# Kernel optimization log

Measured on AMD Instinct MI355X. Metric: run time of the kernel, lower is better.

Reference implementation:

```python
import jax, jax.numpy as jnp
import numpy as np

N_NODES = 20000
N_EDGES = 640000
IN_F = 128
CL1_F = 128
CL2_F = 128
OUT_F = 2


def setup_inputs() -> dict:
    key = jax.random.key(0)
    ks = jax.random.split(key, 8)
    x = jax.random.normal(ks[0], (N_NODES, IN_F), dtype=jnp.float32)
    edge_index = jax.random.randint(ks[1], (2, N_EDGES), 0, N_NODES, dtype=jnp.int64)
    s1 = 1.0 / np.sqrt(IN_F)
    s2 = 1.0 / np.sqrt(CL1_F)
    s3 = 1.0 / np.sqrt(CL2_F)
    W1 = jax.random.uniform(ks[2], (IN_F, CL1_F), jnp.float32, -s1, s1)
    b1 = jax.random.uniform(ks[3], (CL1_F,), jnp.float32, -s1, s1)
    W2 = jax.random.uniform(ks[4], (CL1_F, CL2_F), jnp.float32, -s2, s2)
    b2 = jax.random.uniform(ks[5], (CL2_F,), jnp.float32, -s2, s2)
    W3 = jax.random.uniform(ks[6], (CL2_F, OUT_F), jnp.float32, -s3, s3)
    b3 = jax.random.uniform(ks[7], (OUT_F,), jnp.float32, -s3, s3)
    return {"x": x, "edge_index": edge_index, "W1": W1, "b1": b1,
            "W2": W2, "b2": b2, "W3": W3, "b3": b3}


def _scatter_mean(feat_src, src, dst, n_nodes):
    # out[i] = mean over edges e with dst[e]==i of feat_src gathered at src[e]
    msg = feat_src[src]                                   # [E, F] gather
    summed = jax.ops.segment_sum(msg, dst, num_segments=n_nodes)  # [N, F]
    ones = jnp.ones((src.shape[0],), dtype=feat_src.dtype)
    cnt = jax.ops.segment_sum(ones, dst, num_segments=n_nodes)    # [N]
    return summed / jnp.maximum(cnt, 1.0)[:, None]


def _mpnn_layer(x, src, dst, W, b, n_nodes):
    aggr = _scatter_mean(x, src, dst, n_nodes)
    return jax.nn.relu(aggr @ W + b)


def reference(x, edge_index, W1, b1, W2, b2, W3, b3):
    src, dst = edge_index[0], edge_index[1]
    n = x.shape[0]
    h = _mpnn_layer(x, src, dst, W1, b1, n)   # conv1 (update relu); extra relu is no-op
    h = _mpnn_layer(h, src, dst, W2, b2, n)   # conv2
    # dropout in eval mode is identity
    return h @ W3 + b3
```

## Files before the change

### kernel.cpp

```cpp
#include <hip/hip_runtime.h>

#define N_NODES 20000
#define N_EDGES 640000
#define F 128
#define CAP 128
#define GEMM_BLOCKS (N_NODES / 32)
#define SCAT_BLOCKS 2560
#define QSTRIDE (SCAT_BLOCKS / 8 * 256)
#define NODES_PER_XCD (N_NODES / 8)
#define AGG_BLOCKS 2504


__global__ __launch_bounds__(256)
void gemm_bucket_kernel(const float* __restrict__ A, const float* __restrict__ W,
                        float* __restrict__ C,
                        const int* __restrict__ src, const int* __restrict__ dst,
                        int* __restrict__ cnt, unsigned short* __restrict__ bucket) {
    __shared__ float As[32][F + 4];
    int tid = threadIdx.x;
    int bid = blockIdx.x;

    if (bid >= GEMM_BLOCKS) {
        int s   = bid - GEMM_BLOCKS;
        int g   = bid & 7;
        int idx = s >> 3;
        int lo  = g * NODES_PER_XCD;
        int hi  = lo + NODES_PER_XCD;
        const int4* dst4 = (const int4*)dst;
        const int4* src4 = (const int4*)src;
        for (int q = idx * 256 + tid; q < N_EDGES / 4; q += QSTRIDE) {
            int4 d4 = dst4[q];
            int4 s4 = src4[q];
            if (d4.x >= lo && d4.x < hi) {
                int pos = atomicAdd(&cnt[d4.x], 1);
                if (pos < CAP) bucket[(size_t)d4.x * CAP + pos] = (unsigned short)s4.x;
            }
            if (d4.y >= lo && d4.y < hi) {
                int pos = atomicAdd(&cnt[d4.y], 1);
                if (pos < CAP) bucket[(size_t)d4.y * CAP + pos] = (unsigned short)s4.y;
            }
            if (d4.z >= lo && d4.z < hi) {
                int pos = atomicAdd(&cnt[d4.z], 1);
                if (pos < CAP) bucket[(size_t)d4.z * CAP + pos] = (unsigned short)s4.z;
            }
            if (d4.w >= lo && d4.w < hi) {
                int pos = atomicAdd(&cnt[d4.w], 1);
                if (pos < CAP) bucket[(size_t)d4.w * CAP + pos] = (unsigned short)s4.w;
            }
        }
        return;
    }

    int row0 = bid * 32;
    const float4* A4 = (const float4*)(A + (size_t)row0 * F);
    for (int i = tid; i < 32 * 32; i += 256) {
        float4 v = A4[i];
        int r = i >> 5, c4 = (i & 31) * 4;
        *(float4*)&As[r][c4] = v;
    }
    __syncthreads();

    int tx = tid & 31, ty = tid >> 5;
    int c0 = tx * 4, r0 = ty * 4;
    float acc[4][4] = {};

    for (int k = 0; k < F; k += 4) {
        float4 a4[4];
#pragma unroll
        for (int i = 0; i < 4; ++i) a4[i] = *(const float4*)&As[r0 + i][k];
#pragma unroll
        for (int u = 0; u < 4; ++u) {
            float4 w = *(const float4*)(W + (size_t)(k + u) * F + c0);
#pragma unroll
            for (int i = 0; i < 4; ++i) {
                float a = (u == 0) ? a4[i].x : (u == 1) ? a4[i].y : (u == 2) ? a4[i].z : a4[i].w;
                acc[i][0] += a * w.x;
                acc[i][1] += a * w.y;
                acc[i][2] += a * w.z;
                acc[i][3] += a * w.w;
            }
        }
    }

#pragma unroll
    for (int i = 0; i < 4; ++i) {
        float4 o;
        o.x = acc[i][0]; o.y = acc[i][1]; o.z = acc[i][2]; o.w = acc[i][3];
        *(float4*)(C + (size_t)(row0 + r0 + i) * F + c0) = o;
    }
}

__global__ __launch_bounds__(256)
void gemm_kernel(const float* __restrict__ A, const float* __restrict__ W,
                 float* __restrict__ C) {
    __shared__ float As[32][F + 4];
    int tid  = threadIdx.x;
    int row0 = blockIdx.x * 32;

    const float4* A4 = (const float4*)(A + (size_t)row0 * F);
    for (int i = tid; i < 32 * 32; i += 256) {
        float4 v = A4[i];
        int r = i >> 5, c4 = (i & 31) * 4;
        *(float4*)&As[r][c4] = v;
    }
    __syncthreads();

    int tx = tid & 31, ty = tid >> 5;
    int c0 = tx * 4, r0 = ty * 4;
    float acc[4][4] = {};

    for (int k = 0; k < F; k += 4) {
        float4 a4[4];
#pragma unroll
        for (int i = 0; i < 4; ++i) a4[i] = *(const float4*)&As[r0 + i][k];
#pragma unroll
        for (int u = 0; u < 4; ++u) {
            float4 w = *(const float4*)(W + (size_t)(k + u) * F + c0);
#pragma unroll
            for (int i = 0; i < 4; ++i) {
                float a = (u == 0) ? a4[i].x : (u == 1) ? a4[i].y : (u == 2) ? a4[i].z : a4[i].w;
                acc[i][0] += a * w.x;
                acc[i][1] += a * w.y;
                acc[i][2] += a * w.z;
                acc[i][3] += a * w.w;
            }
        }
    }

#pragma unroll
    for (int i = 0; i < 4; ++i) {
        float4 o;
        o.x = acc[i][0]; o.y = acc[i][1]; o.z = acc[i][2]; o.w = acc[i][3];
        *(float4*)(C + (size_t)(row0 + r0 + i) * F + c0) = o;
    }
}

__global__ __launch_bounds__(256)
void slice_agg_kernel(const float* __restrict__ y, const int* __restrict__ cnt,
                      const unsigned short* __restrict__ bucket,
                      const float* __restrict__ b, float* __restrict__ out) {
    int bid   = blockIdx.x;
    int g     = bid & 7;
    int i     = bid >> 3;
    int slice = g & 3;
    int jj    = i * 2 + (g >> 2);
    int wave  = threadIdx.x >> 6;
    int lane  = threadIdx.x & 63;
    int r     = lane >> 3;
    int c4    = lane & 7;

    int node_base = jj * 32 + wave * 8;
    if (node_base >= N_NODES) return;
    int node = node_base + r;

    int deg = cnt[node];
    int d   = deg < CAP ? deg : CAP;
    const int4* lst4 = (const int4*)(bucket + (size_t)node * CAP);
    const int*  lst  = (const int*)lst4;

    const float4* fb = (const float4*)y + slice * 8 + c4;

    float4 acc0; acc0.x = acc0.y = acc0.z = acc0.w = 0.f;
    float4 acc1; acc1.x = acc1.y = acc1.z = acc1.w = 0.f;
    int c = 0;
    for (; c + 8 <= d; c += 8) {
        int4 w = lst4[c >> 3];
        int i0 = w.x & 0xffff, i1 = (w.x >> 16) & 0xffff;
        int i2 = w.y & 0xffff, i3 = (w.y >> 16) & 0xffff;
        int i4 = w.z & 0xffff, i5 = (w.z >> 16) & 0xffff;
        int i6 = w.w & 0xffff, i7 = (w.w >> 16) & 0xffff;
        float4 v0 = fb[(size_t)i0 * 32];
        float4 v1 = fb[(size_t)i1 * 32];
        float4 v2 = fb[(size_t)i2 * 32];
        float4 v3 = fb[(size_t)i3 * 32];
        float4 v4 = fb[(size_t)i4 * 32];
        float4 v5 = fb[(size_t)i5 * 32];
        float4 v6 = fb[(size_t)i6 * 32];
        float4 v7 = fb[(size_t)i7 * 32];
        acc0.x += (v0.x + v1.x) + (v2.x + v3.x);
        acc0.y += (v0.y + v1.y) + (v2.y + v3.y);
        acc0.z += (v0.z + v1.z) + (v2.z + v3.z);
        acc0.w += (v0.w + v1.w) + (v2.w + v3.w);
        acc1.x += (v4.x + v5.x) + (v6.x + v7.x);
        acc1.y += (v4.y + v5.y) + (v6.y + v7.y);
        acc1.z += (v4.z + v5.z) + (v6.z + v7.z);
        acc1.w += (v4.w + v5.w) + (v6.w + v7.w);
    }
    for (; c < d; ++c) {
        int w   = lst[c >> 1];
        int idx = (c & 1) ? ((w >> 16) & 0xffff) : (w & 0xffff);
        float4 v = fb[(size_t)idx * 32];
        acc0.x += v.x; acc0.y += v.y; acc0.z += v.z; acc0.w += v.w;
    }
    acc0.x += acc1.x; acc0.y += acc1.y; acc0.z += acc1.z; acc0.w += acc1.w;

    float4 bv = ((const float4*)b)[slice * 8 + c4];
    float inv = 1.0f / fmaxf((float)deg, 1.0f);
    float4 o;
    o.x = fmaxf(acc0.x * inv + bv.x, 0.f);
    o.y = fmaxf(acc0.y * inv + bv.y, 0.f);
    o.z = fmaxf(acc0.z * inv + bv.z, 0.f);
    o.w = fmaxf(acc0.w * inv + bv.w, 0.f);
    ((float4*)out)[(size_t)node * 32 + slice * 8 + c4] = o;
}

__global__ __launch_bounds__(256)
void final_kernel(const float* __restrict__ h, const float* __restrict__ W3,
                  const float* __restrict__ b3, float* __restrict__ out) {
    int wid  = (blockIdx.x * blockDim.x + threadIdx.x) >> 6;
    int lane = threadIdx.x & 63;
    if (wid >= N_NODES) return;
    float2 v = ((const float2*)h)[(size_t)wid * 64 + lane];
    float4 w = ((const float4*)W3)[lane];
    float a0 = v.x * w.x + v.y * w.z;
    float a1 = v.x * w.y + v.y * w.w;
#pragma unroll
    for (int off = 32; off > 0; off >>= 1) {
        a0 += __shfl_down(a0, off);
        a1 += __shfl_down(a1, off);
    }
    if (lane == 0) {
        out[(size_t)wid * 2]     = a0 + b3[0];
        out[(size_t)wid * 2 + 1] = a1 + b3[1];
    }
}

extern "C" void kernel_launch(void* const* d_in, const int* in_sizes, int n_in,
                              void* d_out, int out_size, void* d_ws, size_t ws_size,
                              hipStream_t stream) {
    const float* x   = (const float*)d_in[0];
    const int*   ei  = (const int*)d_in[1];
    const int*   src = ei;
    const int*   dst = ei + N_EDGES;
    const float* W1 = (const float*)d_in[2];
    const float* b1 = (const float*)d_in[3];
    const float* W2 = (const float*)d_in[4];
    const float* b2 = (const float*)d_in[5];
    const float* W3 = (const float*)d_in[6];
    const float* b3 = (const float*)d_in[7];
    float* out = (float*)d_out;

    char* base = (char*)d_ws;
    size_t off = 0;
    auto take = [&](size_t bytes) -> char* {
        char* p = base + off;
        off += (bytes + 255) & ~(size_t)255;
        return p;
    };
    int*            cnt    = (int*)           take(N_NODES * sizeof(int));
    unsigned short* bucket = (unsigned short*)take((size_t)N_NODES * CAP * sizeof(unsigned short));
    float*          y      = (float*)         take((size_t)N_NODES * F * sizeof(float));
    float*          h      = (float*)         take((size_t)N_NODES * F * sizeof(float));

    hipMemsetAsync(cnt, 0, N_NODES * sizeof(int), stream);

    gemm_bucket_kernel<<<GEMM_BLOCKS + SCAT_BLOCKS, 256, 0, stream>>>(
        x, W1, y, src, dst, cnt, bucket);
    slice_agg_kernel<<<AGG_BLOCKS, 256, 0, stream>>>(y, cnt, bucket, b1, h);
    gemm_kernel<<<N_NODES / 32, 256, 0, stream>>>(h, W2, y);
    slice_agg_kernel<<<AGG_BLOCKS, 256, 0, stream>>>(y, cnt, bucket, b2, h);
    final_kernel<<<(N_NODES * 64) / 256, 256, 0, stream>>>(h, W3, b3, out);
}
```

Measured before the change: 185.8 us.

## Fuse final projection into second aggregation and halve GEMM row tile

The second aggregation kernel now computes the output projection with W3 directly. Each column slice reduces its partial dot products with shuffles and adds them into the output with atomics, so the h round trip and the separate final kernel go away. The output is zeroed inside the second GEMM, and both GEMMs move to 16-row tiles to launch twice as many blocks. The cost is extra atomic traffic on the output and less register reuse per thread in the GEMM, and float atomics make the summation order nondeterministic.

```diff
diff --git a/kernel.cpp b/kernel.cpp
--- a/kernel.cpp
+++ b/kernel.cpp
@@ -4,7 +4,7 @@
 #define N_EDGES 640000
 #define F 128
 #define CAP 128
-#define GEMM_BLOCKS (N_NODES / 32)
+#define GEMM_BLOCKS (N_NODES / 16)
 #define SCAT_BLOCKS 2560
 #define QSTRIDE (SCAT_BLOCKS / 8 * 256)
 #define NODES_PER_XCD (N_NODES / 8)
@@ -16,7 +16,7 @@
                         float* __restrict__ C,
                         const int* __restrict__ src, const int* __restrict__ dst,
                         int* __restrict__ cnt, unsigned short* __restrict__ bucket) {
-    __shared__ float As[32][F + 4];
+    __shared__ float As[16][F + 4];
     int tid = threadIdx.x;
     int bid = blockIdx.x;
 
@@ -51,9 +51,9 @@
         return;
     }
 
-    int row0 = bid * 32;
+    int row0 = bid * 16;
     const float4* A4 = (const float4*)(A + (size_t)row0 * F);
-    for (int i = tid; i < 32 * 32; i += 256) {
+    for (int i = tid; i < 16 * 32; i += 256) {
         float4 v = A4[i];
         int r = i >> 5, c4 = (i & 31) * 4;
         *(float4*)&As[r][c4] = v;
@@ -61,18 +61,18 @@
     __syncthreads();
 
     int tx = tid & 31, ty = tid >> 5;
-    int c0 = tx * 4, r0 = ty * 4;
-    float acc[4][4] = {};
+    int c0 = tx * 4, r0 = ty * 2;
+    float acc[2][4] = {};
 
     for (int k = 0; k < F; k += 4) {
-        float4 a4[4];
-#pragma unroll
-        for (int i = 0; i < 4; ++i) a4[i] = *(const float4*)&As[r0 + i][k];
+        float4 a4[2];
+#pragma unroll
+        for (int i = 0; i < 2; ++i) a4[i] = *(const float4*)&As[r0 + i][k];
 #pragma unroll
         for (int u = 0; u < 4; ++u) {
             float4 w = *(const float4*)(W + (size_t)(k + u) * F + c0);
 #pragma unroll
-            for (int i = 0; i < 4; ++i) {
+            for (int i = 0; i < 2; ++i) {
                 float a = (u == 0) ? a4[i].x : (u == 1) ? a4[i].y : (u == 2) ? a4[i].z : a4[i].w;
                 acc[i][0] += a * w.x;
                 acc[i][1] += a * w.y;
@@ -83,7 +83,7 @@
     }
 
 #pragma unroll
-    for (int i = 0; i < 4; ++i) {
+    for (int i = 0; i < 2; ++i) {
         float4 o;
         o.x = acc[i][0]; o.y = acc[i][1]; o.z = acc[i][2]; o.w = acc[i][3];
         *(float4*)(C + (size_t)(row0 + r0 + i) * F + c0) = o;
@@ -92,13 +92,19 @@
 
 __global__ __launch_bounds__(256)
 void gemm_kernel(const float* __restrict__ A, const float* __restrict__ W,
-                 float* __restrict__ C) {
-    __shared__ float As[32][F + 4];
+                 float* __restrict__ C, float* __restrict__ outz) {
+    __shared__ float As[16][F + 4];
     int tid  = threadIdx.x;
-    int row0 = blockIdx.x * 32;
+    int row0 = blockIdx.x * 16;
+
+    int t = blockIdx.x * 256 + tid;
+    if (t < (N_NODES * 2) / 4) {
+        float4 z; z.x = z.y = z.z = z.w = 0.f;
+        ((float4*)outz)[t] = z;
+    }
 
     const float4* A4 = (const float4*)(A + (size_t)row0 * F);
-    for (int i = tid; i < 32 * 32; i += 256) {
+    for (int i = tid; i < 16 * 32; i += 256) {
         float4 v = A4[i];
         int r = i >> 5, c4 = (i & 31) * 4;
         *(float4*)&As[r][c4] = v;
@@ -106,18 +112,18 @@
     __syncthreads();
 
     int tx = tid & 31, ty = tid >> 5;
-    int c0 = tx * 4, r0 = ty * 4;
-    float acc[4][4] = {};
+    int c0 = tx * 4, r0 = ty * 2;
+    float acc[2][4] = {};
 
     for (int k = 0; k < F; k += 4) {
-        float4 a4[4];
-#pragma unroll
-        for (int i = 0; i < 4; ++i) a4[i] = *(const float4*)&As[r0 + i][k];
+        float4 a4[2];
+#pragma unroll
+        for (int i = 0; i < 2; ++i) a4[i] = *(const float4*)&As[r0 + i][k];
 #pragma unroll
         for (int u = 0; u < 4; ++u) {
             float4 w = *(const float4*)(W + (size_t)(k + u) * F + c0);
 #pragma unroll
-            for (int i = 0; i < 4; ++i) {
+            for (int i = 0; i < 2; ++i) {
                 float a = (u == 0) ? a4[i].x : (u == 1) ? a4[i].y : (u == 2) ? a4[i].z : a4[i].w;
                 acc[i][0] += a * w.x;
                 acc[i][1] += a * w.y;
@@ -128,7 +134,7 @@
     }
 
 #pragma unroll
-    for (int i = 0; i < 4; ++i) {
+    for (int i = 0; i < 2; ++i) {
         float4 o;
         o.x = acc[i][0]; o.y = acc[i][1]; o.z = acc[i][2]; o.w = acc[i][3];
         *(float4*)(C + (size_t)(row0 + r0 + i) * F + c0) = o;
@@ -205,23 +211,86 @@
 }
 
 __global__ __launch_bounds__(256)
-void final_kernel(const float* __restrict__ h, const float* __restrict__ W3,
-                  const float* __restrict__ b3, float* __restrict__ out) {
-    int wid  = (blockIdx.x * blockDim.x + threadIdx.x) >> 6;
-    int lane = threadIdx.x & 63;
-    if (wid >= N_NODES) return;
-    float2 v = ((const float2*)h)[(size_t)wid * 64 + lane];
-    float4 w = ((const float4*)W3)[lane];
-    float a0 = v.x * w.x + v.y * w.z;
-    float a1 = v.x * w.y + v.y * w.w;
-#pragma unroll
-    for (int off = 32; off > 0; off >>= 1) {
-        a0 += __shfl_down(a0, off);
-        a1 += __shfl_down(a1, off);
-    }
-    if (lane == 0) {
-        out[(size_t)wid * 2]     = a0 + b3[0];
-        out[(size_t)wid * 2 + 1] = a1 + b3[1];
+void agg_final_kernel(const float* __restrict__ y, const int* __restrict__ cnt,
+                      const unsigned short* __restrict__ bucket,
+                      const float* __restrict__ b, const float* __restrict__ W3,
+                      const float* __restrict__ b3, float* __restrict__ out) {
+    int bid   = blockIdx.x;
+    int g     = bid & 7;
+    int i     = bid >> 3;
+    int slice = g & 3;
+    int jj    = i * 2 + (g >> 2);
+    int wave  = threadIdx.x >> 6;
+    int lane  = threadIdx.x & 63;
+    int r     = lane >> 3;
+    int c4    = lane & 7;
+
+    int node_base = jj * 32 + wave * 8;
+    if (node_base >= N_NODES) return;
+    int node = node_base + r;
+
+    int deg = cnt[node];
+    int d   = deg < CAP ? deg : CAP;
+    const int4* lst4 = (const int4*)(bucket + (size_t)node * CAP);
+    const int*  lst  = (const int*)lst4;
+
+    const float4* fb = (const float4*)y + slice * 8 + c4;
+
+    float4 acc0; acc0.x = acc0.y = acc0.z = acc0.w = 0.f;
+    float4 acc1; acc1.x = acc1.y = acc1.z = acc1.w = 0.f;
+    int c = 0;
+    for (; c + 8 <= d; c += 8) {
+        int4 w = lst4[c >> 3];
+        int i0 = w.x & 0xffff, i1 = (w.x >> 16) & 0xffff;
+        int i2 = w.y & 0xffff, i3 = (w.y >> 16) & 0xffff;
+        int i4 = w.z & 0xffff, i5 = (w.z >> 16) & 0xffff;
+        int i6 = w.w & 0xffff, i7 = (w.w >> 16) & 0xffff;
+        float4 v0 = fb[(size_t)i0 * 32];
+        float4 v1 = fb[(size_t)i1 * 32];
+        float4 v2 = fb[(size_t)i2 * 32];
+        float4 v3 = fb[(size_t)i3 * 32];
+        float4 v4 = fb[(size_t)i4 * 32];
+        float4 v5 = fb[(size_t)i5 * 32];
+        float4 v6 = fb[(size_t)i6 * 32];
+        float4 v7 = fb[(size_t)i7 * 32];
+        acc0.x += (v0.x + v1.x) + (v2.x + v3.x);
+        acc0.y += (v0.y + v1.y) + (v2.y + v3.y);
+        acc0.z += (v0.z + v1.z) + (v2.z + v3.z);
+        acc0.w += (v0.w + v1.w) + (v2.w + v3.w);
+        acc1.x += (v4.x + v5.x) + (v6.x + v7.x);
+        acc1.y += (v4.y + v5.y) + (v6.y + v7.y);
+        acc1.z += (v4.z + v5.z) + (v6.z + v7.z);
+        acc1.w += (v4.w + v5.w) + (v6.w + v7.w);
+    }
+    for (; c < d; ++c) {
+        int w   = lst[c >> 1];
+        int idx = (c & 1) ? ((w >> 16) & 0xffff) : (w & 0xffff);
+        float4 v = fb[(size_t)idx * 32];
+        acc0.x += v.x; acc0.y += v.y; acc0.z += v.z; acc0.w += v.w;
+    }
+    acc0.x += acc1.x; acc0.y += acc1.y; acc0.z += acc1.z; acc0.w += acc1.w;
+
+    float4 bv = ((const float4*)b)[slice * 8 + c4];
+    float inv = 1.0f / fmaxf((float)deg, 1.0f);
+    float4 o;
+    o.x = fmaxf(acc0.x * inv + bv.x, 0.f);
+    o.y = fmaxf(acc0.y * inv + bv.y, 0.f);
+    o.z = fmaxf(acc0.z * inv + bv.z, 0.f);
+    o.w = fmaxf(acc0.w * inv + bv.w, 0.f);
+
+    int cc = slice * 32 + c4 * 4;
+    const float4* w3 = (const float4*)W3;
+    float4 wA = w3[cc / 2];
+    float4 wB = w3[cc / 2 + 1];
+    float p0 = o.x * wA.x + o.y * wA.z + o.z * wB.x + o.w * wB.z;
+    float p1 = o.x * wA.y + o.y * wA.w + o.z * wB.y + o.w * wB.w;
+    p0 += __shfl_xor(p0, 1);  p1 += __shfl_xor(p1, 1);
+    p0 += __shfl_xor(p0, 2);  p1 += __shfl_xor(p1, 2);
+    p0 += __shfl_xor(p0, 4);  p1 += __shfl_xor(p1, 4);
+    if (c4 == 0) {
+        if (slice == 0) { p0 += b3[0]; p1 += b3[1]; }
+        atomicAdd(&out[(size_t)node * 2],     p0);
+        atomicAdd(&out[(size_t)node * 2 + 1], p1);
     }
 }
 
@@ -257,7 +326,6 @@
     gemm_bucket_kernel<<<GEMM_BLOCKS + SCAT_BLOCKS, 256, 0, stream>>>(
         x, W1, y, src, dst, cnt, bucket);
     slice_agg_kernel<<<AGG_BLOCKS, 256, 0, stream>>>(y, cnt, bucket, b1, h);
-    gemm_kernel<<<N_NODES / 32, 256, 0, stream>>>(h, W2, y);
-    slice_agg_kernel<<<AGG_BLOCKS, 256, 0, stream>>>(y, cnt, bucket, b2, h);
-    final_kernel<<<(N_NODES * 64) / 256, 256, 0, stream>>>(h, W3, b3, out);
-}
+    gemm_kernel<<<N_NODES / 16, 256, 0, stream>>>(h, W2, y, out);
+    agg_final_kernel<<<AGG_BLOCKS, 256, 0, stream>>>(y, cnt, bucket, b2, W3, b3, out);
+}
```

New measurement: 198.2 us. 1.07x slower.
